# Optimization experiments

Hardware: AMD Instinct MI355X
Metric: run time of the kernel (lower is better)

The kernel has to match this reference:

```python
import jax, jax.numpy as jnp
import numpy as np

NUM_HEADS = 16


def spike(x):
    # forward of SpikeFunction: Heaviside step
    return (x > 0).astype(x.dtype)


def setup_inputs() -> dict:
    key = jax.random.key(0)
    ks = jax.random.split(key, 11)
    B, S, D = 2, 2048, 1024
    s = 1.0 / np.sqrt(D)
    return {
        "query": jax.random.normal(ks[0], (B, S, D), jnp.float32),
        "key": jax.random.normal(ks[1], (B, S, D), jnp.float32),
        "value": jax.random.normal(ks[2], (B, S, D), jnp.float32),
        "Wq": jax.random.normal(ks[3], (D, D), jnp.float32) * s,
        "bq": jnp.zeros((D,), jnp.float32),
        "Wk": jax.random.normal(ks[4], (D, D), jnp.float32) * s,
        "bk": jnp.zeros((D,), jnp.float32),
        "Wv": jax.random.normal(ks[5], (D, D), jnp.float32) * s,
        "bv": jnp.zeros((D,), jnp.float32),
        "Wo": jax.random.normal(ks[6], (D, D), jnp.float32) * s,
        "bo": jnp.zeros((D,), jnp.float32),
    }


def reference(query, key, value, Wq, bq, Wk, bk, Wv, bv, Wo, bo):
    B, S, D = query.shape
    H = NUM_HEADS
    hd = D // H
    # torch Linear: x @ W.T + b
    q = (query @ Wq.T + bq).reshape(B, S, H, hd).transpose(0, 2, 1, 3)
    k = (key @ Wk.T + bk).reshape(B, S, H, hd).transpose(0, 2, 1, 3)
    v = (value @ Wv.T + bv).reshape(B, S, H, hd).transpose(0, 2, 1, 3)
    scale = 1.0 / np.sqrt(hd).astype(np.float32)
    scores = jnp.einsum('bhqd,bhkd->bhqk', q, k) * scale  # [B,H,S,S]
    attn = spike(scores)  # elementwise threshold instead of softmax
    ctx = jnp.einsum('bhqk,bhkd->bhqd', attn, v)
    ctx = ctx.transpose(0, 2, 1, 3).reshape(B, S, D)
    out = ctx @ Wo.T + bo
    return out, attn
```

## Files before the change

kernel.cpp:

```cpp
#include <hip/hip_runtime.h>


#define SEQ 2048
#define DIM 1024
#define NH 16
#define HD 64
#define BATCH 2
#define MROWS (BATCH * SEQ)
#define BHT (BATCH * NH)

typedef __attribute__((ext_vector_type(8))) short short8;
typedef __attribute__((ext_vector_type(4))) float f4;
typedef unsigned short ushort;

__device__ __forceinline__ f4 mfma16(short8 a, short8 b, f4 c) {
    return __builtin_amdgcn_mfma_f32_16x16x32_bf16(a, b, c, 0, 0, 0);
}
__device__ __forceinline__ ushort rne16(float x) {
    union { float f; unsigned u; } a; a.f = x;
    return (ushort)((a.u + 0x7fffu + ((a.u >> 16) & 1u)) >> 16);
}
__device__ __forceinline__ void split2(float x, ushort& h, ushort& l) {
    union { float f; unsigned u; } a; a.f = x;
    unsigned hu = a.u & 0xffff0000u;
    h = (ushort)(hu >> 16);
    union { unsigned u; float f; } hb; hb.u = hu;
    l = rne16(x - hb.f);
}
__device__ __forceinline__ short8 ld8(const ushort* p) { return *(const short8*)p; }

__device__ __forceinline__ void gll16(const ushort* g, ushort* l) {
    __builtin_amdgcn_global_load_lds((const __attribute__((address_space(1))) void*)g,
                                     (__attribute__((address_space(3))) void*)l, 16, 0, 0);
}

__global__ __launch_bounds__(256) void wconv(const float* __restrict__ Wq,
                                             const float* __restrict__ Wk,
                                             const float* __restrict__ Wv,
                                             const float* __restrict__ Wo,
                                             ushort* __restrict__ Wqh, ushort* __restrict__ Wql,
                                             ushort* __restrict__ Wkh, ushort* __restrict__ Wkl,
                                             ushort* __restrict__ Wvb, ushort* __restrict__ Wob) {
    int i = (blockIdx.x * 256 + threadIdx.x) * 4;
    int job = blockIdx.y;
    const float* src = job == 0 ? Wq : job == 1 ? Wk : job == 2 ? Wv : Wo;
    float4 w = *(const float4*)&src[i];
    float xs[4] = {w.x, w.y, w.z, w.w};
    if (job < 2) {
        ushort h[4], l[4];
#pragma unroll
        for (int j = 0; j < 4; ++j) split2(xs[j], h[j], l[j]);
        ushort* ph = job ? Wkh : Wqh;
        ushort* pl = job ? Wkl : Wql;
        *(short4*)&ph[i] = make_short4(h[0], h[1], h[2], h[3]);
        *(short4*)&pl[i] = make_short4(l[0], l[1], l[2], l[3]);
    } else {
        ushort* po = job == 2 ? Wvb : Wob;
        *(short4*)&po[i] = make_short4(rne16(xs[0]), rne16(xs[1]), rne16(xs[2]), rne16(xs[3]));
    }
}

__global__ __launch_bounds__(256, 2) void proj_qkv(
    const float* __restrict__ query, const float* __restrict__ key, const float* __restrict__ value,
    const ushort* __restrict__ Wqh, const ushort* __restrict__ Wql,
    const ushort* __restrict__ Wkh, const ushort* __restrict__ Wkl,
    const ushort* __restrict__ Wvb,
    const float* __restrict__ bq, const float* __restrict__ bk, const float* __restrict__ bv,
    ushort* __restrict__ Qhi, ushort* __restrict__ Qlo,
    ushort* __restrict__ Khi, ushort* __restrict__ Klo, ushort* __restrict__ Vt) {
    __shared__ ushort wst[2][2][64][64];
    __shared__ ushort Ts[4][64][40];
    const int z = blockIdx.z;
    const int t = threadIdx.x, wave = t >> 6, lane = t & 63;
    const int la = lane & 15, qd = lane >> 4;
    const int m0 = blockIdx.x * 128 + wave * 32;
    const int n0 = blockIdx.y * 64;

    const int srow = wave * 16 + (lane >> 3);
    const int schunk = (lane & 7) ^ (lane >> 3);
    const size_t wg0 = (size_t)(n0 + srow) * DIM + schunk * 8;

    if (z < 2) {
        const float* X = z ? key : query;
        const ushort* Wh = z ? Wkh : Wqh;
        const ushort* Wl = z ? Wkl : Wql;

        gll16(&Wh[wg0], &wst[0][0][wave * 16][0]);
        gll16(&Wh[wg0 + 8 * DIM], &wst[0][0][wave * 16 + 8][0]);
        gll16(&Wl[wg0], &wst[0][1][wave * 16][0]);
        gll16(&Wl[wg0 + 8 * DIM], &wst[0][1][wave * 16 + 8][0]);
        __syncthreads();

        f4 acc[2][4] = {};
        for (int k0 = 0; k0 < DIM; k0 += 64) {
            const int cur = (k0 >> 6) & 1;
            float4 xA[2][2][2];
#pragma unroll
            for (int hf = 0; hf < 2; ++hf)
#pragma unroll
                for (int ms = 0; ms < 2; ++ms) {
                    const float* ap = &X[(size_t)(m0 + ms * 16 + la) * DIM + k0 + hf * 32 + qd * 8];
                    xA[hf][ms][0] = *(const float4*)ap;
                    xA[hf][ms][1] = *(const float4*)(ap + 4);
                }
            if (k0 + 64 < DIM) {
                gll16(&Wh[wg0 + k0 + 64], &wst[cur ^ 1][0][wave * 16][0]);
                gll16(&Wh[wg0 + k0 + 64 + 8 * DIM], &wst[cur ^ 1][0][wave * 16 + 8][0]);
                gll16(&Wl[wg0 + k0 + 64], &wst[cur ^ 1][1][wave * 16][0]);
                gll16(&Wl[wg0 + k0 + 64 + 8 * DIM], &wst[cur ^ 1][1][wave * 16 + 8][0]);
            }
#pragma unroll
            for (int hf = 0; hf < 2; ++hf) {
                short8 ahi[2], alo[2];
#pragma unroll
                for (int ms = 0; ms < 2; ++ms) {
                    float xs[8] = {xA[hf][ms][0].x, xA[hf][ms][0].y, xA[hf][ms][0].z,
                                   xA[hf][ms][0].w, xA[hf][ms][1].x, xA[hf][ms][1].y,
                                   xA[hf][ms][1].z, xA[hf][ms][1].w};
#pragma unroll
                    for (int j = 0; j < 8; ++j) {
                        ushort h, l;
                        split2(xs[j], h, l);
                        ahi[ms][j] = (short)h;
                        alo[ms][j] = (short)l;
                    }
                }
#pragma unroll
                for (int ns = 0; ns < 4; ++ns) {
                    int row = ns * 16 + la;
                    int sw = ((hf * 4 + qd) ^ (la & 7)) * 8;
                    short8 wHf = *(const short8*)&wst[cur][0][row][sw];
                    short8 wLf = *(const short8*)&wst[cur][1][row][sw];
#pragma unroll
                    for (int ms = 0; ms < 2; ++ms) {
                        acc[ms][ns] = mfma16(alo[ms], wHf, acc[ms][ns]);
                        acc[ms][ns] = mfma16(ahi[ms], wLf, acc[ms][ns]);
                        acc[ms][ns] = mfma16(ahi[ms], wHf, acc[ms][ns]);
                    }
                }
            }
            __syncthreads();
        }
        const float* bias = z ? bk : bq;
        ushort* Oh = z ? Khi : Qhi;
        ushort* Ol = z ? Klo : Qlo;
#pragma unroll
        for (int ns = 0; ns < 4; ++ns) {
            int n = n0 + ns * 16 + la;
            float bvv = bias[n];
            int h = n >> 6, d = n & 63;
#pragma unroll
            for (int ms = 0; ms < 2; ++ms)
#pragma unroll
                for (int r = 0; r < 4; ++r) {
                    int m = m0 + ms * 16 + qd * 4 + r;
                    int b = m >> 11, s = m & 2047;
                    ushort hh, ll;
                    split2(acc[ms][ns][r] + bvv, hh, ll);
                    size_t o = ((size_t)(b * NH + h) * SEQ + s) * HD + d;
                    __builtin_nontemporal_store(hh, &Oh[o]);
                    __builtin_nontemporal_store(ll, &Ol[o]);
                }
        }
    } else {
        gll16(&Wvb[wg0], &wst[0][0][wave * 16][0]);
        gll16(&Wvb[wg0 + 8 * DIM], &wst[0][0][wave * 16 + 8][0]);
        __syncthreads();

        f4 acc[2][4] = {};
        for (int k0 = 0; k0 < DIM; k0 += 64) {
            const int cur = (k0 >> 6) & 1;
            float4 xA[2][2][2];
#pragma unroll
            for (int hf = 0; hf < 2; ++hf)
#pragma unroll
                for (int ms = 0; ms < 2; ++ms) {
                    const float* ap =
                        &value[(size_t)(m0 + ms * 16 + la) * DIM + k0 + hf * 32 + qd * 8];
                    xA[hf][ms][0] = *(const float4*)ap;
                    xA[hf][ms][1] = *(const float4*)(ap + 4);
                }
            if (k0 + 64 < DIM) {
                gll16(&Wvb[wg0 + k0 + 64], &wst[cur ^ 1][0][wave * 16][0]);
                gll16(&Wvb[wg0 + k0 + 64 + 8 * DIM], &wst[cur ^ 1][0][wave * 16 + 8][0]);
            }
#pragma unroll
            for (int hf = 0; hf < 2; ++hf) {
                short8 a[2];
#pragma unroll
                for (int ms = 0; ms < 2; ++ms) {
                    float xs[8] = {xA[hf][ms][0].x, xA[hf][ms][0].y, xA[hf][ms][0].z,
                                   xA[hf][ms][0].w, xA[hf][ms][1].x, xA[hf][ms][1].y,
                                   xA[hf][ms][1].z, xA[hf][ms][1].w};
#pragma unroll
                    for (int j = 0; j < 8; ++j) a[ms][j] = (short)rne16(xs[j]);
                }
#pragma unroll
                for (int ns = 0; ns < 4; ++ns) {
                    int row = ns * 16 + la;
                    int sw = ((hf * 4 + qd) ^ (la & 7)) * 8;
                    short8 wv = *(const short8*)&wst[cur][0][row][sw];
#pragma unroll
                    for (int ms = 0; ms < 2; ++ms) acc[ms][ns] = mfma16(a[ms], wv, acc[ms][ns]);
                }
            }
            __syncthreads();
        }
#pragma unroll
        for (int ns = 0; ns < 4; ++ns) {
            float bvv = bv[n0 + ns * 16 + la];
#pragma unroll
            for (int ms = 0; ms < 2; ++ms)
#pragma unroll
                for (int r = 0; r < 4; ++r)
                    Ts[wave][ns * 16 + la][ms * 16 + qd * 4 + r] = rne16(acc[ms][ns][r] + bvv);
        }
        int b = m0 >> 11, s0 = m0 & 2047, h = n0 >> 6;
        size_t vbase = (size_t)(b * NH + h) * HD * SEQ;
#pragma unroll
        for (int it = 0; it < 4; ++it) {
            int d = it * 16 + (lane >> 2), sc = (lane & 3) * 8;
            short8 v0 = *(const short8*)&Ts[wave][d][sc];
            __builtin_nontemporal_store(v0, (short8*)&Vt[vbase + (size_t)d * SEQ + s0 + sc]);
        }
    }
}

__global__ __launch_bounds__(256, 4) void attn_mfma(
    const ushort* __restrict__ Qhi, const ushort* __restrict__ Qlo,
    const ushort* __restrict__ Khi, const ushort* __restrict__ Klo,
    const ushort* __restrict__ Vt, float* __restrict__ attn, ushort* __restrict__ ctxb) {
    __shared__ ushort kb[2][2][32][64];
    __shared__ ushort Ps[64][40];
    const int t = threadIdx.x, wave = t >> 6, lane = t & 63;
    const int la = lane & 15, qd = lane >> 4;
    const int bh = blockIdx.x;
    const int q0 = blockIdx.y * 64 + wave * 16;

    short8 qhi[2], qlo[2];
#pragma unroll
    for (int ks = 0; ks < 2; ++ks) {
        size_t qi = ((size_t)bh * SEQ + q0 + la) * HD + ks * 32 + qd * 8;
        qhi[ks] = ld8(&Qhi[qi]);
        qlo[ks] = ld8(&Qlo[qi]);
    }

    const int skey = wave * 8 + (lane >> 3);
    const int schunk = (lane & 7) ^ (lane >> 3);
    const size_t sgbase = ((size_t)bh * SEQ + skey) * HD + schunk * 8;

    gll16(&Khi[sgbase], &kb[0][0][wave * 8][0]);
    gll16(&Klo[sgbase], &kb[0][1][wave * 8][0]);
    __syncthreads();

    f4 cacc[4] = {};
    for (int h = 0; h < 64; ++h) {
        const int c0 = h * 32;
        const int cur = h & 1;

        short8 vB[4];
#pragma unroll
        for (int ns = 0; ns < 4; ++ns)
            vB[ns] = ld8(&Vt[((size_t)bh * HD + ns * 16 + la) * SEQ + c0 + qd * 8]);

        if (h + 1 < 64) {
            gll16(&Khi[sgbase + (size_t)(c0 + 32) * HD], &kb[cur ^ 1][0][wave * 8][0]);
            gll16(&Klo[sgbase + (size_t)(c0 + 32) * HD], &kb[cur ^ 1][1][wave * 8][0]);
        }

        short8 kH[2][2], kL[2][2];
#pragma unroll
        for (int n2 = 0; n2 < 2; ++n2)
#pragma unroll
            for (int ks = 0; ks < 2; ++ks) {
                int row = n2 * 16 + la;
                int sw = ((ks * 4 + qd) ^ (la & 7)) * 8;
                kH[n2][ks] = *(const short8*)&kb[cur][0][row][sw];
                kL[n2][ks] = *(const short8*)&kb[cur][1][row][sw];
            }

        f4 s[2] = {};
        __builtin_amdgcn_s_setprio(1);
#pragma unroll
        for (int n2 = 0; n2 < 2; ++n2)
#pragma unroll
            for (int ks = 0; ks < 2; ++ks) {
                s[n2] = mfma16(qlo[ks], kH[n2][ks], s[n2]);
                s[n2] = mfma16(qhi[ks], kL[n2][ks], s[n2]);
                s[n2] = mfma16(qhi[ks], kH[n2][ks], s[n2]);
            }
        __builtin_amdgcn_s_setprio(0);

#pragma unroll
        for (int n2 = 0; n2 < 2; ++n2)
#pragma unroll
            for (int r = 0; r < 4; ++r)
                Ps[wave * 16 + qd * 4 + r][n2 * 16 + la] =
                    s[n2][r] > 0.f ? (ushort)0x3f80 : (ushort)0;

#pragma unroll
        for (int it = 0; it < 2; ++it) {
            int row = it * 8 + (lane >> 3);
            short4 p = *(const short4*)&Ps[wave * 16 + row][(lane & 7) * 4];
            f4 o;
            o.x = __uint_as_float(((unsigned)(ushort)p.x) << 16);
            o.y = __uint_as_float(((unsigned)(ushort)p.y) << 16);
            o.z = __uint_as_float(((unsigned)(ushort)p.z) << 16);
            o.w = __uint_as_float(((unsigned)(ushort)p.w) << 16);
            __builtin_nontemporal_store(
                o, (f4*)&attn[((size_t)bh * SEQ + q0 + row) * SEQ + c0 + (lane & 7) * 4]);
        }

        short8 pa = *(const short8*)&Ps[wave * 16 + la][qd * 8];
        __builtin_amdgcn_s_setprio(1);
#pragma unroll
        for (int ns = 0; ns < 4; ++ns) cacc[ns] = mfma16(pa, vB[ns], cacc[ns]);
        __builtin_amdgcn_s_setprio(0);

        __syncthreads();
    }
#pragma unroll
    for (int ns = 0; ns < 4; ++ns)
#pragma unroll
        for (int r = 0; r < 4; ++r) {
            int qrow = q0 + qd * 4 + r;
            __builtin_nontemporal_store(rne16(cacc[ns][r]),
                                        &ctxb[((size_t)bh * SEQ + qrow) * HD + ns * 16 + la]);
        }
}

template <int B>
__device__ __forceinline__ void ld_o(const ushort* __restrict__ Ctx, const ushort* __restrict__ Wb,
                                     int m0, int n0, int la, int qd, int k0,
                                     short8 (&aO)[2][2], short8 (&wO)[2][4]) {
#pragma unroll
    for (int ms = 0; ms < 2; ++ms) {
        int m = m0 + ms * 16 + la;
        int b = m >> 11, s = m & 2047;
        int k = k0 + qd * 8;
        int h = k >> 6, d = k & 63;
        aO[B][ms] = ld8(&Ctx[((size_t)(b * NH + h) * SEQ + s) * HD + d]);
    }
#pragma unroll
    for (int ns = 0; ns < 4; ++ns)
        wO[B][ns] = ld8(&Wb[(size_t)(n0 + ns * 16 + la) * DIM + k0 + qd * 8]);
}

__global__ __launch_bounds__(256, 2) void proj_out(const ushort* __restrict__ Ctx,
                                                   const ushort* __restrict__ Wb,
                                                   const float* __restrict__ bias,
                                                   float* __restrict__ out) {
    const int t = threadIdx.x, wave = t >> 6, lane = t & 63;
    const int la = lane & 15, qd = lane >> 4;
    const int m0 = blockIdx.x * 128 + wave * 32;
    const int n0 = blockIdx.y * 64;

    short8 aO[2][2], wO[2][4];
    f4 acc[2][4] = {};
    ld_o<0>(Ctx, Wb, m0, n0, la, qd, 0, aO, wO);
    for (int k0 = 0; k0 < DIM; k0 += 64) {
        ld_o<1>(Ctx, Wb, m0, n0, la, qd, k0 + 32, aO, wO);
#pragma unroll
        for (int ns = 0; ns < 4; ++ns)
#pragma unroll
            for (int ms = 0; ms < 2; ++ms) acc[ms][ns] = mfma16(aO[0][ms], wO[0][ns], acc[ms][ns]);
        ld_o<0>(Ctx, Wb, m0, n0, la, qd, (k0 + 64) & (DIM - 1), aO, wO);
#pragma unroll
        for (int ns = 0; ns < 4; ++ns)
#pragma unroll
            for (int ms = 0; ms < 2; ++ms) acc[ms][ns] = mfma16(aO[1][ms], wO[1][ns], acc[ms][ns]);
    }
#pragma unroll
    for (int ns = 0; ns < 4; ++ns) {
        int n = n0 + ns * 16 + la;
        float bvv = bias[n];
#pragma unroll
        for (int ms = 0; ms < 2; ++ms)
#pragma unroll
            for (int r = 0; r < 4; ++r) {
                int m = m0 + ms * 16 + qd * 4 + r;
                __builtin_nontemporal_store(acc[ms][ns][r] + bvv, &out[(size_t)m * DIM + n]);
            }
    }
}

extern "C" void kernel_launch(void* const* d_in, const int* in_sizes, int n_in,
                              void* d_out, int out_size, void* d_ws, size_t ws_size,
                              hipStream_t stream) {
    const float* query = (const float*)d_in[0];
    const float* key   = (const float*)d_in[1];
    const float* value = (const float*)d_in[2];
    const float* Wq = (const float*)d_in[3];
    const float* bq = (const float*)d_in[4];
    const float* Wk = (const float*)d_in[5];
    const float* bk = (const float*)d_in[6];
    const float* Wv = (const float*)d_in[7];
    const float* bv = (const float*)d_in[8];
    const float* Wo = (const float*)d_in[9];
    const float* bo = (const float*)d_in[10];

    float* out  = (float*)d_out;
    float* attn = out + (size_t)MROWS * DIM;

    const size_t NE = (size_t)MROWS * DIM;
    const size_t WE = (size_t)DIM * DIM;
    ushort* Qhi = (ushort*)d_ws;
    ushort* Qlo = Qhi + NE;
    ushort* Khi = Qlo + NE;
    ushort* Klo = Khi + NE;
    ushort* Vt  = Klo + NE;
    ushort* Wqh = Vt + NE;
    ushort* Wql = Wqh + WE;
    ushort* Wkh = Wql + WE;
    ushort* Wkl = Wkh + WE;
    ushort* Wvb = Wkl + WE;
    ushort* Wob = Wvb + WE;
    ushort* Ctx = Wqh;

    dim3 blk(256);
    hipLaunchKernelGGL(wconv, dim3(WE / 1024, 4), blk, 0, stream,
                       Wq, Wk, Wv, Wo, Wqh, Wql, Wkh, Wkl, Wvb, Wob);
    hipLaunchKernelGGL(proj_qkv, dim3(32, 16, 3), blk, 0, stream,
                       query, key, value, Wqh, Wql, Wkh, Wkl, Wvb, bq, bk, bv,
                       Qhi, Qlo, Khi, Klo, Vt);
    hipLaunchKernelGGL(attn_mfma, dim3(32, 32), blk, 0, stream,
                       Qhi, Qlo, Khi, Klo, Vt, attn, Ctx);
    hipLaunchKernelGGL(proj_out, dim3(32, 16), blk, 0, stream, Ctx, Wob, bo, out);
}
```

Measured before the change: 903.2 us.

## Stage output-projection weights through double-buffered swizzled LDS in proj_out

The output projection kernel now loads each 64x64 weight tile once per block into shared memory with direct global-to-LDS loads, double-buffered across k-steps and XOR-swizzled to avoid bank conflicts. Previously each of the four waves fetched the same weight fragments from global memory on its own. Context fragments are still read from global per wave. The change adds a block barrier every k-step and gives up the previous register-level prefetch of the activations.

```diff
diff --git a/kernel.cpp b/kernel.cpp
--- a/kernel.cpp
+++ b/kernel.cpp
@@ -329,46 +329,53 @@
         }
 }
 
-template <int B>
-__device__ __forceinline__ void ld_o(const ushort* __restrict__ Ctx, const ushort* __restrict__ Wb,
-                                     int m0, int n0, int la, int qd, int k0,
-                                     short8 (&aO)[2][2], short8 (&wO)[2][4]) {
-#pragma unroll
-    for (int ms = 0; ms < 2; ++ms) {
-        int m = m0 + ms * 16 + la;
-        int b = m >> 11, s = m & 2047;
-        int k = k0 + qd * 8;
-        int h = k >> 6, d = k & 63;
-        aO[B][ms] = ld8(&Ctx[((size_t)(b * NH + h) * SEQ + s) * HD + d]);
-    }
-#pragma unroll
-    for (int ns = 0; ns < 4; ++ns)
-        wO[B][ns] = ld8(&Wb[(size_t)(n0 + ns * 16 + la) * DIM + k0 + qd * 8]);
-}
-
 __global__ __launch_bounds__(256, 2) void proj_out(const ushort* __restrict__ Ctx,
                                                    const ushort* __restrict__ Wb,
                                                    const float* __restrict__ bias,
                                                    float* __restrict__ out) {
+    __shared__ ushort wst[2][64][64];
     const int t = threadIdx.x, wave = t >> 6, lane = t & 63;
     const int la = lane & 15, qd = lane >> 4;
     const int m0 = blockIdx.x * 128 + wave * 32;
     const int n0 = blockIdx.y * 64;
 
-    short8 aO[2][2], wO[2][4];
+    const int srow = wave * 16 + (lane >> 3);
+    const int schunk = (lane & 7) ^ (lane >> 3);
+    const size_t wg0 = (size_t)(n0 + srow) * DIM + schunk * 8;
+
+    gll16(&Wb[wg0], &wst[0][wave * 16][0]);
+    gll16(&Wb[wg0 + 8 * DIM], &wst[0][wave * 16 + 8][0]);
+    __syncthreads();
+
     f4 acc[2][4] = {};
-    ld_o<0>(Ctx, Wb, m0, n0, la, qd, 0, aO, wO);
     for (int k0 = 0; k0 < DIM; k0 += 64) {
-        ld_o<1>(Ctx, Wb, m0, n0, la, qd, k0 + 32, aO, wO);
-#pragma unroll
-        for (int ns = 0; ns < 4; ++ns)
-#pragma unroll
-            for (int ms = 0; ms < 2; ++ms) acc[ms][ns] = mfma16(aO[0][ms], wO[0][ns], acc[ms][ns]);
-        ld_o<0>(Ctx, Wb, m0, n0, la, qd, (k0 + 64) & (DIM - 1), aO, wO);
-#pragma unroll
-        for (int ns = 0; ns < 4; ++ns)
-#pragma unroll
-            for (int ms = 0; ms < 2; ++ms) acc[ms][ns] = mfma16(aO[1][ms], wO[1][ns], acc[ms][ns]);
+        const int cur = (k0 >> 6) & 1;
+        const int hsel = k0 >> 6;
+        short8 aO[2][2];
+#pragma unroll
+        for (int hf = 0; hf < 2; ++hf)
+#pragma unroll
+            for (int ms = 0; ms < 2; ++ms) {
+                int m = m0 + ms * 16 + la;
+                int b = m >> 11, s = m & 2047;
+                aO[hf][ms] =
+                    ld8(&Ctx[((size_t)(b * NH + hsel) * SEQ + s) * HD + hf * 32 + qd * 8]);
+            }
+        if (k0 + 64 < DIM) {
+            gll16(&Wb[wg0 + k0 + 64], &wst[cur ^ 1][wave * 16][0]);
+            gll16(&Wb[wg0 + k0 + 64 + 8 * DIM], &wst[cur ^ 1][wave * 16 + 8][0]);
+        }
+#pragma unroll
+        for (int hf = 0; hf < 2; ++hf)
+#pragma unroll
+            for (int ns = 0; ns < 4; ++ns) {
+                int row = ns * 16 + la;
+                int sw = ((hf * 4 + qd) ^ (la & 7)) * 8;
+                short8 wv = *(const short8*)&wst[cur][row][sw];
+#pragma unroll
+                for (int ms = 0; ms < 2; ++ms) acc[ms][ns] = mfma16(aO[hf][ms], wv, acc[ms][ns]);
+            }
+        __syncthreads();
     }
 #pragma unroll
     for (int ns = 0; ns < 4; ++ns) {
```

Measured after the change: 881.5 us. 2.4% less time.
